# Kernel tuning notes

Measured on AMD Instinct MI355X. Metric: run time of the kernel, lower is better.

Reference implementation:

```python
import jax, jax.numpy as jnp
import numpy as np

B = 524288   # batch rows
K = 8        # number of BooleanClassifiers
I = 64       # n_inputs
H = 32       # n_hidden
SCALE = 1.0  # LinearNetwork.scale (default [1.0])


def setup_inputs() -> dict:
    key = jax.random.key(0)
    k_x, k_w1, k_b1, k_w2, k_b2 = jax.random.split(key, 5)
    return {
        "x": jax.random.normal(k_x, (B, I), dtype=jnp.float32),
        "W1": jax.random.normal(k_w1, (K, H, I), dtype=jnp.float32) * 0.1,
        "b1": jax.random.normal(k_b1, (K, H), dtype=jnp.float32) * 0.1,
        "W2": jax.random.normal(k_w2, (K, H), dtype=jnp.float32) * 0.1,
        "b2": jax.random.normal(k_b2, (K,), dtype=jnp.float32) * 0.1,
        "bias": jnp.zeros((K,), dtype=jnp.float32),  # unused in training-mode forward
    }


def reference(x, W1, b1, W2, b2, bias):
    # Loop of K tiny Linear-Tanh-Linear-Tanh classifiers, fused as batched GEMMs.
    # h: [B, K, H]
    h = jnp.tanh(jnp.einsum("bi,khi->bkh", x, W1) + b1)
    # per-classifier scalar output, concatenated along dim=1 -> [B, K]
    out = jnp.tanh(jnp.einsum("bkh,kh->bk", h, W2) + b2)
    out = out * SCALE                   # LinearNetwork scale
    out = (out + 1.0) * 0.5 * SCALE     # LinearWithTanh training branch
    return out
```

## Files before the change

kernel.cpp:

```cpp
#include <hip/hip_runtime.h>

typedef __attribute__((ext_vector_type(8))) short short8;
typedef __attribute__((ext_vector_type(4))) float f32x4;

constexpr int B_ROWS   = 524288;
constexpr int ROWTILES = B_ROWS / 64;
constexpr int GRID     = 2048;
constexpr int ITERS    = ROWTILES / GRID;
constexpr float L2E2   = 2.8853900817779268f;

union V16 { uint4 u; short8 s; };

__device__ __forceinline__ unsigned pk(float lo, float hi) {
  const unsigned a = __float_as_uint(lo) + 0x8000u;
  const unsigned b = __float_as_uint(hi) + 0x8000u;
  return __builtin_amdgcn_perm(b, a, 0x07060302u);
}

__device__ __forceinline__ V16 pk8(f32x4 a, f32x4 b) {
  V16 v;
  v.u.x = pk(a[0], a[1]); v.u.y = pk(a[2], a[3]);
  v.u.z = pk(b[0], b[1]); v.u.w = pk(b[2], b[3]);
  return v;
}

__global__ __launch_bounds__(512, 4) void fused_mlp8(
    const float* __restrict__ x, const float* __restrict__ W1,
    const float* __restrict__ b1, const float* __restrict__ W2,
    const float* __restrict__ b2, float* __restrict__ out) {

  __shared__ V16 xb[2][512];

  const int tid  = threadIdx.x;
  const int wave = tid >> 6;
  const int lane = tid & 63;
  const int m16  = lane & 15;
  const int q    = lane >> 4;

  const int srow = tid >> 3;
  const int seg  = tid & 7;
  const int sw   = srow & 7;
  const float* gbase = x + (long)srow * 64 + seg * 8;

  f32x4 pf0 = *(const f32x4*)(gbase + (long)blockIdx.x * 4096);
  f32x4 pf1 = *(const f32x4*)(gbase + (long)blockIdx.x * 4096 + 4);

  short8 w1f[2][2];
#pragma unroll
  for (int mt = 0; mt < 2; ++mt) {
    const int n = wave * 32 + mt * 16 + m16;
#pragma unroll
    for (int ks = 0; ks < 2; ++ks) {
      const float* p = W1 + n * 64 + ks * 32 + q * 8;
      const f32x4 u0 = *(const f32x4*)p, u1 = *(const f32x4*)(p + 4);
      f32x4 s0, s1;
#pragma unroll
      for (int r = 0; r < 4; ++r) { s0[r] = L2E2 * u0[r]; s1[r] = L2E2 * u1[r]; }
      w1f[mt][ks] = pk8(s0, s1).s;
    }
  }

  f32x4 kb1[2], w2q[2];
  float s = 0.f;
#pragma unroll
  for (int mt = 0; mt < 2; ++mt) {
    const int n0 = wave * 32 + mt * 16 + q * 4;
    const f32x4 b1x = *(const f32x4*)(b1 + n0);
    const f32x4 w2x = *(const f32x4*)(W2 + n0);
#pragma unroll
    for (int r = 0; r < 4; ++r) {
      kb1[mt][r] = L2E2 * b1x[r];
      w2q[mt][r] = (2.0f * L2E2) * w2x[r];
      s += w2x[r];
    }
  }
  s += __shfl_xor(s, 16);
  s += __shfl_xor(s, 32);
  const float KSbn = -0.25f * L2E2 * (s + b2[wave]);

  xb[0][srow * 8 + (seg ^ sw)] = pk8(pf0, pf1);
  pf0 = *(const f32x4*)(gbase + ((long)blockIdx.x + GRID) * 4096);
  pf1 = *(const f32x4*)(gbase + ((long)blockIdx.x + GRID) * 4096 + 4);
  __syncthreads();

#pragma unroll
  for (int i = 0; i < ITERS; ++i) {
    const int p = i & 1;
    const long tile = (long)blockIdx.x + (long)i * GRID;

    float osel = 0.f;
#pragma unroll
    for (int tt = 0; tt < 4; ++tt) {
      const int r   = tt * 16 + m16;
      const int rsw = r & 7;
      const short8 xf0 = xb[p][r * 8 + (q       ^ rsw)].s;
      const short8 xf1 = xb[p][r * 8 + ((q + 4) ^ rsw)].s;

      f32x4 acc[2];
#pragma unroll
      for (int mt = 0; mt < 2; ++mt) {
        f32x4 z = kb1[mt];
        z = __builtin_amdgcn_mfma_f32_16x16x32_bf16(w1f[mt][0], xf0, z, 0, 0, 0);
        z = __builtin_amdgcn_mfma_f32_16x16x32_bf16(w1f[mt][1], xf1, z, 0, 0, 0);
        acc[mt] = z;
      }

      float P = KSbn;
#pragma unroll
      for (int mt = 0; mt < 2; ++mt) {
        const float e0 = __builtin_amdgcn_exp2f(acc[mt][0]);
        const float e1 = __builtin_amdgcn_exp2f(acc[mt][1]);
        const float e2 = __builtin_amdgcn_exp2f(acc[mt][2]);
        const float e3 = __builtin_amdgcn_exp2f(acc[mt][3]);
        const float f0 = e0 + 1.0f, f1 = e1 + 1.0f;
        const float f2 = e2 + 1.0f, f3 = e3 + 1.0f;
        const float p01 = f0 * f1, p23 = f2 * f3;
        const float n01 = __builtin_fmaf(w2q[mt][0], f1, w2q[mt][1] * f0);
        const float n23 = __builtin_fmaf(w2q[mt][2], f3, w2q[mt][3] * f2);
        const float N   = __builtin_fmaf(n01, p23, n23 * p01);
        P = __builtin_fmaf(N, __builtin_amdgcn_rcpf(p01 * p23), P);
      }
      P += __shfl_xor(P, 16);
      P += __shfl_xor(P, 32);
      const float o = __builtin_amdgcn_rcpf(__builtin_amdgcn_exp2f(P) + 1.0f);
      osel = (tt == q) ? o : osel;
    }

    out[(tile * 64 + lane) * 8 + wave] = osel;

    if (i + 1 < ITERS) {
      xb[p ^ 1][srow * 8 + (seg ^ sw)] = pk8(pf0, pf1);
    }

    __syncthreads();

    if (i + 2 < ITERS) {
      const float* gp = gbase + (tile + 2 * GRID) * 4096;
      pf0 = *(const f32x4*)gp;
      pf1 = *(const f32x4*)(gp + 4);
    }
  }
}

extern "C" void kernel_launch(void* const* d_in, const int* in_sizes, int n_in,
                              void* d_out, int out_size, void* d_ws, size_t ws_size,
                              hipStream_t stream) {
  const float* x  = (const float*)d_in[0];
  const float* W1 = (const float*)d_in[1];
  const float* b1 = (const float*)d_in[2];
  const float* W2 = (const float*)d_in[3];
  const float* b2 = (const float*)d_in[4];
  float* out = (float*)d_out;
  fused_mlp8<<<GRID, 512, 0, stream>>>(x, W1, b1, W2, b2, out);
}
```

Before: 209.4 us.

## Load x fragments directly into registers per wave, removing LDS staging and barriers

Each wave now loads its own MFMA B-operand fragments of x straight from global memory into registers, converts them to bf16 in registers, and double-buffers the loads one 16-row step ahead. The shared-memory tile, swizzle and per-iteration __syncthreads are gone. Blocks also take contiguous row tiles instead of grid-strided ones. In exchange, all 8 waves in a block read the same x rows, so x traffic goes up 8x at the L1/L2 level, and each lane's loads are less coalesced.

```diff
diff --git a/kernel.cpp b/kernel.cpp
--- a/kernel.cpp
+++ b/kernel.cpp
@@ -3,11 +3,9 @@
 typedef __attribute__((ext_vector_type(8))) short short8;
 typedef __attribute__((ext_vector_type(4))) float f32x4;
 
-constexpr int B_ROWS   = 524288;
-constexpr int ROWTILES = B_ROWS / 64;
-constexpr int GRID     = 2048;
-constexpr int ITERS    = ROWTILES / GRID;
-constexpr float L2E2   = 2.8853900817779268f;
+constexpr int ITERS = 4;
+constexpr int GRID  = 2048;
+constexpr float L2E2 = 2.8853900817779268f;
 
 union V16 { uint4 u; short8 s; };
 
@@ -17,11 +15,11 @@
   return __builtin_amdgcn_perm(b, a, 0x07060302u);
 }
 
-__device__ __forceinline__ V16 pk8(f32x4 a, f32x4 b) {
+__device__ __forceinline__ short8 pk8(f32x4 a, f32x4 b) {
   V16 v;
   v.u.x = pk(a[0], a[1]); v.u.y = pk(a[2], a[3]);
   v.u.z = pk(b[0], b[1]); v.u.w = pk(b[2], b[3]);
-  return v;
+  return v.s;
 }
 
 __global__ __launch_bounds__(512, 4) void fused_mlp8(
@@ -29,21 +27,20 @@
     const float* __restrict__ b1, const float* __restrict__ W2,
     const float* __restrict__ b2, float* __restrict__ out) {
 
-  __shared__ V16 xb[2][512];
-
   const int tid  = threadIdx.x;
   const int wave = tid >> 6;
   const int lane = tid & 63;
   const int m16  = lane & 15;
   const int q    = lane >> 4;
 
-  const int srow = tid >> 3;
-  const int seg  = tid & 7;
-  const int sw   = srow & 7;
-  const float* gbase = x + (long)srow * 64 + seg * 8;
+  const float* xl = x + (long)blockIdx.x * (ITERS * 64 * 64) + m16 * 64 + q * 8;
 
-  f32x4 pf0 = *(const f32x4*)(gbase + (long)blockIdx.x * 4096);
-  f32x4 pf1 = *(const f32x4*)(gbase + (long)blockIdx.x * 4096 + 4);
+  f32x4 ld[2][4];
+#pragma unroll
+  for (int c = 0; c < 2; ++c) {
+    ld[0][2 * c]     = *(const f32x4*)(xl + c * 32);
+    ld[0][2 * c + 1] = *(const f32x4*)(xl + c * 32 + 4);
+  }
 
   short8 w1f[2][2];
 #pragma unroll
@@ -56,7 +53,7 @@
       f32x4 s0, s1;
 #pragma unroll
       for (int r = 0; r < 4; ++r) { s0[r] = L2E2 * u0[r]; s1[r] = L2E2 * u1[r]; }
-      w1f[mt][ks] = pk8(s0, s1).s;
+      w1f[mt][ks] = pk8(s0, s1);
     }
   }
 
@@ -78,66 +75,57 @@
   s += __shfl_xor(s, 32);
   const float KSbn = -0.25f * L2E2 * (s + b2[wave]);
 
-  xb[0][srow * 8 + (seg ^ sw)] = pk8(pf0, pf1);
-  pf0 = *(const f32x4*)(gbase + ((long)blockIdx.x + GRID) * 4096);
-  pf1 = *(const f32x4*)(gbase + ((long)blockIdx.x + GRID) * 4096 + 4);
-  __syncthreads();
+  float osel = 0.f;
+#pragma unroll
+  for (int st = 0; st < ITERS * 4; ++st) {
+    const int i  = st >> 2;
+    const int tt = st & 3;
+    const int cur = st & 1;
 
+    if (st + 1 < ITERS * 4) {
+      const float* gp = xl + (st + 1) * 1024;
 #pragma unroll
-  for (int i = 0; i < ITERS; ++i) {
-    const int p = i & 1;
-    const long tile = (long)blockIdx.x + (long)i * GRID;
-
-    float osel = 0.f;
-#pragma unroll
-    for (int tt = 0; tt < 4; ++tt) {
-      const int r   = tt * 16 + m16;
-      const int rsw = r & 7;
-      const short8 xf0 = xb[p][r * 8 + (q       ^ rsw)].s;
-      const short8 xf1 = xb[p][r * 8 + ((q + 4) ^ rsw)].s;
-
-      f32x4 acc[2];
-#pragma unroll
-      for (int mt = 0; mt < 2; ++mt) {
-        f32x4 z = kb1[mt];
-        z = __builtin_amdgcn_mfma_f32_16x16x32_bf16(w1f[mt][0], xf0, z, 0, 0, 0);
-        z = __builtin_amdgcn_mfma_f32_16x16x32_bf16(w1f[mt][1], xf1, z, 0, 0, 0);
-        acc[mt] = z;
+      for (int c = 0; c < 2; ++c) {
+        ld[cur ^ 1][2 * c]     = *(const f32x4*)(gp + c * 32);
+        ld[cur ^ 1][2 * c + 1] = *(const f32x4*)(gp + c * 32 + 4);
       }
-
-      float P = KSbn;
-#pragma unroll
-      for (int mt = 0; mt < 2; ++mt) {
-        const float e0 = __builtin_amdgcn_exp2f(acc[mt][0]);
-        const float e1 = __builtin_amdgcn_exp2f(acc[mt][1]);
-        const float e2 = __builtin_amdgcn_exp2f(acc[mt][2]);
-        const float e3 = __builtin_amdgcn_exp2f(acc[mt][3]);
-        const float f0 = e0 + 1.0f, f1 = e1 + 1.0f;
-        const float f2 = e2 + 1.0f, f3 = e3 + 1.0f;
-        const float p01 = f0 * f1, p23 = f2 * f3;
-        const float n01 = __builtin_fmaf(w2q[mt][0], f1, w2q[mt][1] * f0);
-        const float n23 = __builtin_fmaf(w2q[mt][2], f3, w2q[mt][3] * f2);
-        const float N   = __builtin_fmaf(n01, p23, n23 * p01);
-        P = __builtin_fmaf(N, __builtin_amdgcn_rcpf(p01 * p23), P);
-      }
-      P += __shfl_xor(P, 16);
-      P += __shfl_xor(P, 32);
-      const float o = __builtin_amdgcn_rcpf(__builtin_amdgcn_exp2f(P) + 1.0f);
-      osel = (tt == q) ? o : osel;
     }
 
-    out[(tile * 64 + lane) * 8 + wave] = osel;
+    const short8 xf0 = pk8(ld[cur][0], ld[cur][1]);
+    const short8 xf1 = pk8(ld[cur][2], ld[cur][3]);
 
-    if (i + 1 < ITERS) {
-      xb[p ^ 1][srow * 8 + (seg ^ sw)] = pk8(pf0, pf1);
+    f32x4 acc[2];
+#pragma unroll
+    for (int mt = 0; mt < 2; ++mt) {
+      f32x4 z = kb1[mt];
+      z = __builtin_amdgcn_mfma_f32_16x16x32_bf16(w1f[mt][0], xf0, z, 0, 0, 0);
+      z = __builtin_amdgcn_mfma_f32_16x16x32_bf16(w1f[mt][1], xf1, z, 0, 0, 0);
+      acc[mt] = z;
     }
 
-    __syncthreads();
+    float P = KSbn;
+#pragma unroll
+    for (int mt = 0; mt < 2; ++mt) {
+      const float e0 = __builtin_amdgcn_exp2f(acc[mt][0]);
+      const float e1 = __builtin_amdgcn_exp2f(acc[mt][1]);
+      const float e2 = __builtin_amdgcn_exp2f(acc[mt][2]);
+      const float e3 = __builtin_amdgcn_exp2f(acc[mt][3]);
+      const float f0 = e0 + 1.0f, f1 = e1 + 1.0f;
+      const float f2 = e2 + 1.0f, f3 = e3 + 1.0f;
+      const float p01 = f0 * f1, p23 = f2 * f3;
+      const float n01 = __builtin_fmaf(w2q[mt][0], f1, w2q[mt][1] * f0);
+      const float n23 = __builtin_fmaf(w2q[mt][2], f3, w2q[mt][3] * f2);
+      const float N   = __builtin_fmaf(n01, p23, n23 * p01);
+      P = __builtin_fmaf(N, __builtin_amdgcn_rcpf(p01 * p23), P);
+    }
+    P += __shfl_xor(P, 16);
+    P += __shfl_xor(P, 32);
+    const float o = __builtin_amdgcn_rcpf(__builtin_amdgcn_exp2f(P) + 1.0f);
+    osel = (tt == q) ? o : osel;
 
-    if (i + 2 < ITERS) {
-      const float* gp = gbase + (tile + 2 * GRID) * 4096;
-      pf0 = *(const f32x4*)gp;
-      pf1 = *(const f32x4*)(gp + 4);
+    if (tt == 3) {
+      const long tile = (long)blockIdx.x * ITERS + i;
+      out[(tile * 64 + lane) * 8 + wave] = osel;
     }
   }
 }
```

Measured after the change: 287.5 us. +37.3%, slower.

## Split classifiers across block pairs with smaller blocks and grid-stride tiles

Applied to the files above, without the earlier changes.

Each block now handles four of the eight classifiers using 256 threads, and two blocks share each row tile, so x is read and converted once per block in the pair. The grid becomes 1792 blocks with a per-block tile count instead of a fixed unrolled trip count. The aim is finer-grained scheduling and better CU balance and occupancy. The cost is duplicated x loads and bf16 packing, plus a non-unrolled loop.

```diff
diff --git a/kernel.cpp b/kernel.cpp
--- a/kernel.cpp
+++ b/kernel.cpp
@@ -3,11 +3,10 @@
 typedef __attribute__((ext_vector_type(8))) short short8;
 typedef __attribute__((ext_vector_type(4))) float f32x4;
 
-constexpr int B_ROWS   = 524288;
-constexpr int ROWTILES = B_ROWS / 64;
-constexpr int GRID     = 2048;
-constexpr int ITERS    = ROWTILES / GRID;
-constexpr float L2E2   = 2.8853900817779268f;
+constexpr int NTILES = 8192;
+constexpr int GRID   = 1792;
+constexpr int PAIRS  = GRID / 2;
+constexpr float L2E2 = 2.8853900817779268f;
 
 union V16 { uint4 u; short8 s; };
 
@@ -24,7 +23,7 @@
   return v;
 }
 
-__global__ __launch_bounds__(512, 4) void fused_mlp8(
+__global__ __launch_bounds__(256, 4) void fused_mlp8(
     const float* __restrict__ x, const float* __restrict__ W1,
     const float* __restrict__ b1, const float* __restrict__ W2,
     const float* __restrict__ b2, float* __restrict__ out) {
@@ -37,18 +36,27 @@
   const int m16  = lane & 15;
   const int q    = lane >> 4;
 
-  const int srow = tid >> 3;
-  const int seg  = tid & 7;
+  const int khalf = blockIdx.x & 1;
+  const int tbase = blockIdx.x >> 1;
+  const int nt    = (NTILES - tbase + PAIRS - 1) / PAIRS;
+  const int k     = khalf * 4 + wave;
+
+  const int srow = tid >> 2;
+  const int seg  = tid & 3;
   const int sw   = srow & 7;
-  const float* gbase = x + (long)srow * 64 + seg * 8;
+  const float* gbase = x + (long)srow * 64 + seg * 16;
 
-  f32x4 pf0 = *(const f32x4*)(gbase + (long)blockIdx.x * 4096);
-  f32x4 pf1 = *(const f32x4*)(gbase + (long)blockIdx.x * 4096 + 4);
+  f32x4 pf[4];
+  {
+    const float* gp = gbase + (long)tbase * 4096;
+#pragma unroll
+    for (int c = 0; c < 4; ++c) pf[c] = *(const f32x4*)(gp + c * 4);
+  }
 
   short8 w1f[2][2];
 #pragma unroll
   for (int mt = 0; mt < 2; ++mt) {
-    const int n = wave * 32 + mt * 16 + m16;
+    const int n = k * 32 + mt * 16 + m16;
 #pragma unroll
     for (int ks = 0; ks < 2; ++ks) {
       const float* p = W1 + n * 64 + ks * 32 + q * 8;
@@ -64,7 +72,7 @@
   float s = 0.f;
 #pragma unroll
   for (int mt = 0; mt < 2; ++mt) {
-    const int n0 = wave * 32 + mt * 16 + q * 4;
+    const int n0 = k * 32 + mt * 16 + q * 4;
     const f32x4 b1x = *(const f32x4*)(b1 + n0);
     const f32x4 w2x = *(const f32x4*)(W2 + n0);
 #pragma unroll
@@ -76,17 +84,20 @@
   }
   s += __shfl_xor(s, 16);
   s += __shfl_xor(s, 32);
-  const float KSbn = -0.25f * L2E2 * (s + b2[wave]);
+  const float KSbn = -0.25f * L2E2 * (s + b2[k]);
 
-  xb[0][srow * 8 + (seg ^ sw)] = pk8(pf0, pf1);
-  pf0 = *(const f32x4*)(gbase + ((long)blockIdx.x + GRID) * 4096);
-  pf1 = *(const f32x4*)(gbase + ((long)blockIdx.x + GRID) * 4096 + 4);
+  xb[0][srow * 8 + ((seg * 2)     ^ sw)] = pk8(pf[0], pf[1]);
+  xb[0][srow * 8 + ((seg * 2 + 1) ^ sw)] = pk8(pf[2], pf[3]);
+  if (nt > 1) {
+    const float* gp = gbase + ((long)tbase + PAIRS) * 4096;
+#pragma unroll
+    for (int c = 0; c < 4; ++c) pf[c] = *(const f32x4*)(gp + c * 4);
+  }
   __syncthreads();
 
-#pragma unroll
-  for (int i = 0; i < ITERS; ++i) {
+  for (int i = 0; i < nt; ++i) {
     const int p = i & 1;
-    const long tile = (long)blockIdx.x + (long)i * GRID;
+    const long tile = tbase + (long)i * PAIRS;
 
     float osel = 0.f;
 #pragma unroll
@@ -126,18 +137,19 @@
       osel = (tt == q) ? o : osel;
     }
 
-    out[(tile * 64 + lane) * 8 + wave] = osel;
+    out[(tile * 64 + lane) * 8 + k] = osel;
 
-    if (i + 1 < ITERS) {
-      xb[p ^ 1][srow * 8 + (seg ^ sw)] = pk8(pf0, pf1);
+    if (i + 1 < nt) {
+      xb[p ^ 1][srow * 8 + ((seg * 2)     ^ sw)] = pk8(pf[0], pf[1]);
+      xb[p ^ 1][srow * 8 + ((seg * 2 + 1) ^ sw)] = pk8(pf[2], pf[3]);
     }
 
     __syncthreads();
 
-    if (i + 2 < ITERS) {
-      const float* gp = gbase + (tile + 2 * GRID) * 4096;
-      pf0 = *(const f32x4*)gp;
-      pf1 = *(const f32x4*)(gp + 4);
+    if (i + 2 < nt) {
+      const float* gp = gbase + (tile + 2 * PAIRS) * 4096;
+#pragma unroll
+      for (int c = 0; c < 4; ++c) pf[c] = *(const f32x4*)(gp + c * 4);
     }
   }
 }
@@ -151,5 +163,5 @@
   const float* W2 = (const float*)d_in[3];
   const float* b2 = (const float*)d_in[4];
   float* out = (float*)d_out;
-  fused_mlp8<<<GRID, 512, 0, stream>>>(x, W1, b1, W2, b2, out);
+  fused_mlp8<<<GRID, 256, 0, stream>>>(x, W1, b1, W2, b2, out);
 }
```

After: 210.6 us. No clear change (+0.6%).
